# Kernel tuning notes

Measured on AMD Instinct MI355X. Metric: run time of the kernel, lower is better.

The kernel has to match this reference:

```python
import jax, jax.numpy as jnp
import numpy as np

NUM_TAGS = 64
SOS_IDX, EOS_IDX, PAD_IDX = 1, 2, 0
NEG = -10000.0


def _make_trans(key):
    t = np.array(jax.random.normal(key, (NUM_TAGS, NUM_TAGS), dtype=jnp.float32))
    t[SOS_IDX, :] = NEG
    t[:, EOS_IDX] = NEG
    t[:, PAD_IDX] = NEG
    t[PAD_IDX, :] = NEG
    t[PAD_IDX, EOS_IDX] = 0.0
    t[PAD_IDX, PAD_IDX] = 0.0
    return jnp.asarray(t)


def setup_inputs() -> dict:
    key = jax.random.key(0)
    k_h, k_len, k_tr = jax.random.split(key, 3)
    B, T = 256, 1024
    h = jax.random.normal(k_h, (B, T, NUM_TAGS), dtype=jnp.float32)
    # variable-length prefix mask (1.0 for valid steps)
    lengths = jax.random.randint(k_len, (B,), 1, T + 1)
    mask = (jnp.arange(T)[None, :] < lengths[:, None]).astype(jnp.float32)
    trans = _make_trans(k_tr)
    return {"h": h, "mask": mask, "trans": trans}


def reference(h, mask, trans):
    # h: [B, T, N] emissions; mask: [B, T]; trans: [N_next, N_prev]
    B, T, N = h.shape
    init = jnp.full((B, N), NEG, dtype=h.dtype).at[:, SOS_IDX].set(0.0)

    def step(score, xs):
        h_t, m_t = xs  # [B, N], [B]
        # score[b, prev] + emit[b, next] + trans[next, prev] -> lse over prev
        s = score[:, None, :] + h_t[:, :, None] + trans[None, :, :]
        new = jax.nn.logsumexp(s, axis=-1)  # [B, N]
        m = m_t[:, None]
        score = new * m + score * (1.0 - m)
        return score, None

    score, _ = jax.lax.scan(step, init, (jnp.swapaxes(h, 0, 1), mask.T))
    # terminal transition to EOS, then partition function per batch element
    return jax.nn.logsumexp(score + trans[EOS_IDX][None, :], axis=-1)  # [B]
```

## Files before the change

### kernel.cpp

```cpp
#include <hip/hip_runtime.h>

#define BATCH 256
#define TT 1024
#define NN 64
#define CHUNK 64
#define NCH 16
#define SOS 1
#define EOSI 2
#define LN2F 0.6931471805599453f
#define LOG2E 1.4426950408889634f

typedef short bf16x8 __attribute__((ext_vector_type(8)));
typedef float f32x4 __attribute__((ext_vector_type(4)));

__device__ __forceinline__ unsigned short f2bf(float x) {
  unsigned u = __float_as_uint(x);
  u += 0x7fffu + ((u >> 16) & 1u);
  return (unsigned short)(u >> 16);
}
__device__ __forceinline__ float bf2f(unsigned short v) { return __uint_as_float(((unsigned)v) << 16); }
__device__ __forceinline__ unsigned cvtpk(float lo, float hi) {
  unsigned r;
  asm("v_cvt_pk_bf16_f32 %0, %1, %2" : "=v"(r) : "v"(lo), "v"(hi));
  return r;
}

__device__ __forceinline__ int padr(int k, int c) {
  return ((k >> 5) << 10) + (((k >> 3) & 3) << 8) + (c << 4) + ((k & 7) << 1);
}

__device__ __forceinline__ int wave_len(const float* mask, int b, int l) {
  float ls = 0.f;
#pragma unroll
  for (int c = 0; c < 4; ++c) {
    float4 m4 = *reinterpret_cast<const float4*>(mask + (size_t)b * TT + c * 256 + l * 4);
    ls += (m4.x + m4.y) + (m4.z + m4.w);
  }
#pragma unroll
  for (int m = 1; m < 64; m <<= 1) ls += __shfl_xor(ls, m, 64);
  return (int)(ls + 0.5f);
}

__global__ __launch_bounds__(256, 4) void crf_chunk(const float* __restrict__ h,
                                                    const float* __restrict__ mask,
                                                    const float* __restrict__ trans,
                                                    unsigned short* __restrict__ mats,
                                                    int* __restrict__ scalesI) {
  __shared__ __align__(16) char lds[4 * 2048 + 4 * 256];
  const int tid = threadIdx.x;
  const int w = tid >> 6, l = tid & 63;
  const int h4 = l >> 4, cl = l & 15;
  const int cp = blockIdx.x >> 8;
  const int b = blockIdx.x & (BATCH - 1);

  char* P = lds + w * 2048;
  char* ehB = lds + 8192 + w * 256;
  const int wp = 2 * (16 * ((l >> 2) & 3) + 4 * (l >> 4) + (l & 3));

  const int len = wave_len(mask, b, l);

  bf16x8 ef[4][2];
#pragma unroll
  for (int I = 0; I < 4; ++I)
#pragma unroll
    for (int Kc = 0; Kc < 2; ++Kc) {
      const float* p = trans + (16 * I + cl) * 64 + 32 * Kc + 8 * h4;
      bf16x8 v;
#pragma unroll
      for (int e = 0; e < 8; ++e) v[e] = (short)f2bf(__expf(p[e]));
      ef[I][Kc] = v;
    }

  for (int half = 0; half < 2; ++half) {
    const int c = half ? (NCH - 1 - cp) : cp;
    const int t0 = c * CHUNK;
    if (t0 >= len) continue;
    const int nstep = min(CHUNK, len - t0);

#pragma unroll
    for (int i = 0; i < 2; ++i) *(f32x4*)(P + ((i * 64 + l) << 4)) = f32x4{0.f, 0.f, 0.f, 0.f};
    if (l < 16) *(unsigned short*)(P + padr(16 * w + l, l)) = 0x3F80;

    const float* hb = h + ((size_t)b * TT + t0) * NN + l;
    *(unsigned short*)(ehB + wp) = f2bf(exp2f(hb[0] * LOG2E));
    uint4 ua = *(uint4*)(ehB + 32 * h4);
    uint4 ub = *(uint4*)(ehB + 32 * h4 + 16);
    float hvN = hb[(size_t)min(1, nstep - 1) * NN];
    float hvN2 = hb[(size_t)min(2, nstep - 1) * NN];
    asm volatile("" ::: "memory");

    int esum = 0, ePend = 0;
    int pp = 128;
    uint4 uaN = ua, ubN = ub;

    for (int t = 0; t < nstep; ++t) {
      if (t + 1 < nstep) {
        const int ec = (((t + 1) & 3) == 0) ? ePend : 0;
        esum += ec;
        *(unsigned short*)(ehB + pp + wp) = f2bf(exp2f(fmaf(hvN, LOG2E, (float)(-ec))));
        uaN = *(uint4*)(ehB + pp + 32 * h4);
        ubN = *(uint4*)(ehB + pp + 32 * h4 + 16);
        hvN = hvN2;
        hvN2 = hb[(size_t)min(t + 3, nstep - 1) * NN];
      }
      bf16x8 fc0 = *(bf16x8*)(P + (l << 4));
      bf16x8 fc1 = *(bf16x8*)(P + 1024 + (l << 4));
      f32x4 a[4];
#pragma unroll
      for (int I = 0; I < 4; ++I) a[I] = f32x4{0.f, 0.f, 0.f, 0.f};
#pragma unroll
      for (int I = 0; I < 4; ++I) {
        a[I] = __builtin_amdgcn_mfma_f32_16x16x32_bf16(ef[I][0], fc0, a[I], 0, 0, 0);
        a[I] = __builtin_amdgcn_mfma_f32_16x16x32_bf16(ef[I][1], fc1, a[I], 0, 0, 0);
      }
      const bool meas = ((t & 3) == 2);
      float prox = 0.f;
#pragma unroll
      for (int I = 0; I < 4; ++I) {
        const unsigned d0 = (I == 0) ? ua.x : (I == 1) ? ua.z : (I == 2) ? ub.x : ub.z;
        const unsigned d1 = (I == 0) ? ua.y : (I == 1) ? ua.w : (I == 2) ? ub.y : ub.w;
        f32x4 eh = {__uint_as_float(d0 << 16), __uint_as_float(d0 & 0xffff0000u),
                    __uint_as_float(d1 << 16), __uint_as_float(d1 & 0xffff0000u)};
        f32x4 v = a[I] * eh;
        if (meas) prox = fmaxf(prox, fmaxf(fmaxf(v[0], v[1]), fmaxf(v[2], v[3])));
        *(uint2*)(P + padr(16 * I + 4 * h4, cl)) = uint2{cvtpk(v[0], v[1]), cvtpk(v[2], v[3])};
      }
      if (meas) {
        prox = fmaxf(prox, __shfl_xor(prox, 16, 64));
        prox = fmaxf(prox, __shfl_xor(prox, 32, 64));
        const float px = __int_as_float(__builtin_amdgcn_readlane(__float_as_int(prox), 5));
        ePend = (__float_as_int(px) >> 23) - 127;
      }
      ua = uaN;
      ub = ubN;
      pp ^= 128;
      asm volatile("" ::: "memory");
    }

    const float scF = __int_as_float((127 - ePend) << 23);
    esum += ePend;
    unsigned short* gm = mats + (size_t)(b * NCH + c) * 4096 + l * 64 + 16 * w;
    unsigned q[8];
#pragma unroll
    for (int p = 0; p < 8; ++p) {
      float x0 = bf2f(*(unsigned short*)(P + padr(l, 2 * p))) * scF;
      float x1 = bf2f(*(unsigned short*)(P + padr(l, 2 * p + 1))) * scF;
      q[p] = cvtpk(x0, x1);
    }
    *(uint4*)gm = uint4{q[0], q[1], q[2], q[3]};
    *(uint4*)(gm + 8) = uint4{q[4], q[5], q[6], q[7]};
    if (l == 0) scalesI[(b * NCH + c) * 4 + w] = esum;
    asm volatile("" ::: "memory");
  }
}

__global__ __launch_bounds__(64) void crf_fold(const float* __restrict__ mask,
                                               const float* __restrict__ trans,
                                               const unsigned short* __restrict__ mats,
                                               const int* __restrict__ scalesI,
                                               float* __restrict__ out) {
  __shared__ float pv[NN];
  const int l = threadIdx.x;
  const int b = blockIdx.x;
  const int len = wave_len(mask, b, l);
  const int nc = (len + CHUNK - 1) / CHUNK;

  float pr = (l == SOS) ? 1.f : 0.f;
  int eA = 0;
  long esumT = 0;

  for (int c = 0; c < nc; ++c) {
    const int* sI = scalesI + (b * NCH + c) * 4;
    const int e0 = sI[0], e1 = sI[1], e2 = sI[2], e3 = sI[3];
    const int S = max(max(e0, e1), max(e2, e3));
    const int g = l >> 4;
    int dl = (g == 0) ? e0 : (g == 1) ? e1 : (g == 2) ? e2 : e3;
    dl -= S;
    pv[l] = ldexpf(pr, dl - eA);
    asm volatile("" ::: "memory");
    esumT += S + eA;

    const uint4* Mr = (const uint4*)(mats + (size_t)(b * NCH + c) * 4096 + l * 64);
    uint4 U[8];
#pragma unroll
    for (int j = 0; j < 8; ++j) U[j] = Mr[j];
    float ac0 = 0.f, ac1 = 0.f, ac2 = 0.f, ac3 = 0.f;
#pragma unroll
    for (int j = 0; j < 8; ++j) {
      f32x4 pa = *(f32x4*)(pv + j * 8);
      f32x4 pb = *(f32x4*)(pv + j * 8 + 4);
      uint4 qq = U[j];
      ac0 = fmaf(__uint_as_float(qq.x << 16), pa[0], ac0);
      ac1 = fmaf(__uint_as_float(qq.x & 0xffff0000u), pa[1], ac1);
      ac2 = fmaf(__uint_as_float(qq.y << 16), pa[2], ac2);
      ac3 = fmaf(__uint_as_float(qq.y & 0xffff0000u), pa[3], ac3);
      ac0 = fmaf(__uint_as_float(qq.z << 16), pb[0], ac0);
      ac1 = fmaf(__uint_as_float(qq.z & 0xffff0000u), pb[1], ac1);
      ac2 = fmaf(__uint_as_float(qq.w << 16), pb[2], ac2);
      ac3 = fmaf(__uint_as_float(qq.w & 0xffff0000u), pb[3], ac3);
    }
    pr = (ac0 + ac1) + (ac2 + ac3);
    float mm = pr;
#pragma unroll
    for (int m = 1; m < 64; m <<= 1) mm = fmaxf(mm, __shfl_xor(mm, m, 64));
    eA = (__float_as_int(mm) >> 23) - 127;
    asm volatile("" ::: "memory");
  }

  float s = pr * __expf(trans[EOSI * NN + l]);
#pragma unroll
  for (int m = 1; m < 64; m <<= 1) s += __shfl_xor(s, m, 64);
  if (l == 0) out[b] = __logf(s) + LN2F * (float)esumT;
}

extern "C" void kernel_launch(void* const* d_in, const int* in_sizes, int n_in,
                              void* d_out, int out_size, void* d_ws, size_t ws_size,
                              hipStream_t stream) {
  const float* h = (const float*)d_in[0];
  const float* mask = (const float*)d_in[1];
  const float* trans = (const float*)d_in[2];
  float* out = (float*)d_out;

  unsigned short* mats = (unsigned short*)d_ws;
  int* scalesI = (int*)((char*)d_ws + (size_t)BATCH * NCH * 4096 * 2);

  hipLaunchKernelGGL(crf_chunk, dim3(BATCH * 8), dim3(256), 0, stream, h, mask, trans, mats, scalesI);
  hipLaunchKernelGGL(crf_fold, dim3(BATCH), dim3(64), 0, stream, mask, trans, mats, scalesI, out);
}
```

Baseline: 182.2 us.

## Compute full 64x64 chunk transfer matrix in one wave instead of four

Each block previously used four waves, each propagating a 16-column slice of the chunk's 64x64 transfer matrix. Now one 64-thread wave handles all 64 columns, looping over four column groups per timestep and prefetching the next group's B fragments from LDS. The redundant per-wave work is removed: each wave no longer recomputes the emission exponentials, the exp(trans) fragments or the mask length. In exchange each wave's serial per-step dependency chain becomes four times longer, and the launch has a quarter as many threads.

```diff
diff --git a/kernel.cpp b/kernel.cpp
--- a/kernel.cpp
+++ b/kernel.cpp
@@ -25,8 +25,8 @@
   return r;
 }
 
-__device__ __forceinline__ int padr(int k, int c) {
-  return ((k >> 5) << 10) + (((k >> 3) & 3) << 8) + (c << 4) + ((k & 7) << 1);
+__device__ __forceinline__ int tadr(int k, int c) {
+  return ((c >> 4) << 11) + ((k >> 5) << 10) + (((k >> 3) & 3) << 8) + ((c & 15) << 4) + ((k & 7) << 1);
 }
 
 __device__ __forceinline__ int wave_len(const float* mask, int b, int l) {
@@ -41,20 +41,18 @@
   return (int)(ls + 0.5f);
 }
 
-__global__ __launch_bounds__(256, 4) void crf_chunk(const float* __restrict__ h,
-                                                    const float* __restrict__ mask,
-                                                    const float* __restrict__ trans,
-                                                    unsigned short* __restrict__ mats,
-                                                    int* __restrict__ scalesI) {
-  __shared__ __align__(16) char lds[4 * 2048 + 4 * 256];
-  const int tid = threadIdx.x;
-  const int w = tid >> 6, l = tid & 63;
+__global__ __launch_bounds__(64, 4) void crf_chunk(const float* __restrict__ h,
+                                                   const float* __restrict__ mask,
+                                                   const float* __restrict__ trans,
+                                                   unsigned short* __restrict__ mats,
+                                                   int* __restrict__ scalesI) {
+  __shared__ __align__(16) char lds[8192 + 256];
+  char* P = lds;
+  char* ehB = lds + 8192;
+  const int l = threadIdx.x;
   const int h4 = l >> 4, cl = l & 15;
   const int cp = blockIdx.x >> 8;
   const int b = blockIdx.x & (BATCH - 1);
-
-  char* P = lds + w * 2048;
-  char* ehB = lds + 8192 + w * 256;
   const int wp = 2 * (16 * ((l >> 2) & 3) + 4 * (l >> 4) + (l & 3));
 
   const int len = wave_len(mask, b, l);
@@ -78,8 +76,8 @@
     const int nstep = min(CHUNK, len - t0);
 
 #pragma unroll
-    for (int i = 0; i < 2; ++i) *(f32x4*)(P + ((i * 64 + l) << 4)) = f32x4{0.f, 0.f, 0.f, 0.f};
-    if (l < 16) *(unsigned short*)(P + padr(16 * w + l, l)) = 0x3F80;
+    for (int i = 0; i < 8; ++i) *(f32x4*)(P + ((i * 64 + l) << 4)) = f32x4{0.f, 0.f, 0.f, 0.f};
+    *(unsigned short*)(P + tadr(l, l)) = 0x3F80;
 
     const float* hb = h + ((size_t)b * TT + t0) * NN + l;
     *(unsigned short*)(ehB + wp) = f2bf(exp2f(hb[0] * LOG2E));
@@ -103,27 +101,41 @@
         hvN = hvN2;
         hvN2 = hb[(size_t)min(t + 3, nstep - 1) * NN];
       }
-      bf16x8 fc0 = *(bf16x8*)(P + (l << 4));
-      bf16x8 fc1 = *(bf16x8*)(P + 1024 + (l << 4));
-      f32x4 a[4];
-#pragma unroll
-      for (int I = 0; I < 4; ++I) a[I] = f32x4{0.f, 0.f, 0.f, 0.f};
-#pragma unroll
-      for (int I = 0; I < 4; ++I) {
-        a[I] = __builtin_amdgcn_mfma_f32_16x16x32_bf16(ef[I][0], fc0, a[I], 0, 0, 0);
-        a[I] = __builtin_amdgcn_mfma_f32_16x16x32_bf16(ef[I][1], fc1, a[I], 0, 0, 0);
-      }
-      const bool meas = ((t & 3) == 2);
-      float prox = 0.f;
+      f32x4 eh4[4];
 #pragma unroll
       for (int I = 0; I < 4; ++I) {
         const unsigned d0 = (I == 0) ? ua.x : (I == 1) ? ua.z : (I == 2) ? ub.x : ub.z;
         const unsigned d1 = (I == 0) ? ua.y : (I == 1) ? ua.w : (I == 2) ? ub.y : ub.w;
-        f32x4 eh = {__uint_as_float(d0 << 16), __uint_as_float(d0 & 0xffff0000u),
-                    __uint_as_float(d1 << 16), __uint_as_float(d1 & 0xffff0000u)};
-        f32x4 v = a[I] * eh;
-        if (meas) prox = fmaxf(prox, fmaxf(fmaxf(v[0], v[1]), fmaxf(v[2], v[3])));
-        *(uint2*)(P + padr(16 * I + 4 * h4, cl)) = uint2{cvtpk(v[0], v[1]), cvtpk(v[2], v[3])};
+        eh4[I] = f32x4{__uint_as_float(d0 << 16), __uint_as_float(d0 & 0xffff0000u),
+                       __uint_as_float(d1 << 16), __uint_as_float(d1 & 0xffff0000u)};
+      }
+      const bool meas = ((t & 3) == 2);
+      float prox = 0.f;
+      bf16x8 fc0 = *(bf16x8*)(P + (l << 4));
+      bf16x8 fc1 = *(bf16x8*)(P + 1024 + (l << 4));
+#pragma unroll
+      for (int J = 0; J < 4; ++J) {
+        bf16x8 fn0, fn1;
+        if (J < 3) {
+          fn0 = *(bf16x8*)(P + (2 * J + 2) * 1024 + (l << 4));
+          fn1 = *(bf16x8*)(P + (2 * J + 3) * 1024 + (l << 4));
+        }
+        f32x4 a[4];
+#pragma unroll
+        for (int I = 0; I < 4; ++I) a[I] = f32x4{0.f, 0.f, 0.f, 0.f};
+#pragma unroll
+        for (int I = 0; I < 4; ++I) {
+          a[I] = __builtin_amdgcn_mfma_f32_16x16x32_bf16(ef[I][0], fc0, a[I], 0, 0, 0);
+          a[I] = __builtin_amdgcn_mfma_f32_16x16x32_bf16(ef[I][1], fc1, a[I], 0, 0, 0);
+        }
+#pragma unroll
+        for (int I = 0; I < 4; ++I) {
+          f32x4 v = a[I] * eh4[I];
+          if (meas && J == 0) prox = fmaxf(prox, fmaxf(fmaxf(v[0], v[1]), fmaxf(v[2], v[3])));
+          *(uint2*)(P + tadr(16 * I + 4 * h4, 16 * J + cl)) = uint2{cvtpk(v[0], v[1]), cvtpk(v[2], v[3])};
+        }
+        fc0 = fn0;
+        fc1 = fn1;
       }
       if (meas) {
         prox = fmaxf(prox, __shfl_xor(prox, 16, 64));
@@ -139,17 +151,19 @@
 
     const float scF = __int_as_float((127 - ePend) << 23);
     esum += ePend;
-    unsigned short* gm = mats + (size_t)(b * NCH + c) * 4096 + l * 64 + 16 * w;
-    unsigned q[8];
-#pragma unroll
-    for (int p = 0; p < 8; ++p) {
-      float x0 = bf2f(*(unsigned short*)(P + padr(l, 2 * p))) * scF;
-      float x1 = bf2f(*(unsigned short*)(P + padr(l, 2 * p + 1))) * scF;
-      q[p] = cvtpk(x0, x1);
-    }
-    *(uint4*)gm = uint4{q[0], q[1], q[2], q[3]};
-    *(uint4*)(gm + 8) = uint4{q[4], q[5], q[6], q[7]};
-    if (l == 0) scalesI[(b * NCH + c) * 4 + w] = esum;
+    unsigned short* gm = mats + (size_t)(b * NCH + c) * 4096;
+#pragma unroll
+    for (int j0 = 0; j0 < 64; j0 += 8) {
+      unsigned q[4];
+#pragma unroll
+      for (int p = 0; p < 4; ++p) {
+        float x0 = bf2f(*(unsigned short*)(P + tadr(l, j0 + 2 * p))) * scF;
+        float x1 = bf2f(*(unsigned short*)(P + tadr(l, j0 + 2 * p + 1))) * scF;
+        q[p] = cvtpk(x0, x1);
+      }
+      *(uint4*)(gm + l * 64 + j0) = uint4{q[0], q[1], q[2], q[3]};
+    }
+    if (l < 4) scalesI[(b * NCH + c) * 4 + l] = esum;
     asm volatile("" ::: "memory");
   }
 }
@@ -224,6 +238,6 @@
   unsigned short* mats = (unsigned short*)d_ws;
   int* scalesI = (int*)((char*)d_ws + (size_t)BATCH * NCH * 4096 * 2);
 
-  hipLaunchKernelGGL(crf_chunk, dim3(BATCH * 8), dim3(256), 0, stream, h, mask, trans, mats, scalesI);
+  hipLaunchKernelGGL(crf_chunk, dim3(8 * BATCH), dim3(64), 0, stream, h, mask, trans, mats, scalesI);
   hipLaunchKernelGGL(crf_fold, dim3(BATCH), dim3(64), 0, stream, mask, trans, mats, scalesI, out);
 }
```

Result: faster. 171.1 us (-6.1%).
